# Kernel tuning notes

Measured on AMD Instinct MI355X. Metric: run time of the kernel, lower is better.

Reference implementation:

```python
import jax, jax.numpy as jnp
import numpy as np

N_NODES = 100000
N_EDGES = 3200000
F_IN = 256
N_CLASSES = 10


def setup_inputs() -> dict:
    key = jax.random.key(0)
    ks = jax.random.split(key, 10)
    x = jax.random.normal(ks[0], (N_NODES, F_IN), dtype=jnp.float32)
    edge_index = jax.random.randint(ks[1], (2, N_EDGES), 0, N_NODES, dtype=jnp.int64)
    def glorot(k, fan_in, fan_out):
        s = (6.0 / (fan_in + fan_out)) ** 0.5
        return jax.random.uniform(k, (fan_in, fan_out), jnp.float32, -s, s)
    return {
        "x": x,
        "edge_index": edge_index,
        "W_gcn": glorot(ks[2], F_IN, 64),
        "b_gcn": jnp.zeros((64,), jnp.float32),
        "W1": glorot(ks[3], 64, 32),
        "b1": jnp.zeros((32,), jnp.float32),
        "W2": glorot(ks[4], 32, 16),
        "b2": jnp.zeros((16,), jnp.float32),
        "W3": glorot(ks[5], 16, N_CLASSES),
        "b3": jnp.zeros((N_CLASSES,), jnp.float32),
    }


def gcn_conv(x, edge_index, W, b):
    # PyG GCNConv: x' = D^{-1/2} (A + I) D^{-1/2} (x W) + b, with self-loops.
    n = x.shape[0]
    loop = jnp.arange(n, dtype=edge_index.dtype)
    src = jnp.concatenate([edge_index[0], loop])  # [E+N]
    dst = jnp.concatenate([edge_index[1], loop])
    deg = jax.ops.segment_sum(jnp.ones(src.shape, jnp.float32), dst, num_segments=n)
    dinv = jnp.where(deg > 0, jax.lax.rsqrt(deg), 0.0)
    norm = dinv[src] * dinv[dst]  # [E+N]
    h = x @ W  # transform first (reduces message width to 64)
    msg = h[src] * norm[:, None]  # gather + scale
    out = jax.ops.segment_sum(msg, dst, num_segments=n)  # scatter-add
    return out + b


def reference(x, edge_index, W_gcn, b_gcn, W1, b1, W2, b2, W3, b3):
    # Dropout is a no-op in eval mode; reference uses deterministic eval math.
    h = jax.nn.relu(gcn_conv(x, edge_index, W_gcn, b_gcn))
    h = jax.nn.relu(h @ W1 + b1)
    h = jax.nn.relu(h @ W2 + b2)
    return h @ W3 + b3
```

## Files before the change

kernel.cpp:

```cpp
#include <hip/hip_runtime.h>

#define F_IN 256
#define CHUNK 8192

typedef short bf8_t __attribute__((ext_vector_type(8)));
typedef float f4_t  __attribute__((ext_vector_type(4)));

__device__ __forceinline__ unsigned short f2bf(float f) {
  unsigned u = __float_as_uint(f);
  unsigned r = (u + 0x7FFFu + ((u >> 16) & 1u)) >> 16;
  return (unsigned short)r;
}
#define BF_LO(d) __uint_as_float((d) << 16)
#define BF_HI(d) __uint_as_float((d) & 0xFFFF0000u)

__device__ __forceinline__ bf8_t pack8(float4 a, float4 b) {
  bf8_t r;
  r[0] = (short)f2bf(a.x); r[1] = (short)f2bf(a.y);
  r[2] = (short)f2bf(a.z); r[3] = (short)f2bf(a.w);
  r[4] = (short)f2bf(b.x); r[5] = (short)f2bf(b.y);
  r[6] = (short)f2bf(b.z); r[7] = (short)f2bf(b.w);
  return r;
}

__global__ __launch_bounds__(256) void wprep_kernel(
    const float* __restrict__ W, unsigned short* __restrict__ WbT) {
  const int i = blockIdx.x * 256 + threadIdx.x;
  const int k = i >> 6, n = i & 63;
  WbT[n * 256 + k] = f2bf(W[i]);
}

__global__ __launch_bounds__(256) void gemm_direct_kernel(
    const float* __restrict__ x, const unsigned short* __restrict__ WbT,
    const float* __restrict__ dinvp, unsigned short* __restrict__ hb, int M) {
  __shared__ short Bs[64][264];
  const int t = threadIdx.x;
  for (int i = t; i < 2048; i += 256) {
    const int n = i >> 5, kq = (i & 31) << 3;
    *(uint4*)&Bs[n][kq] = *(const uint4*)(WbT + n * 256 + kq);
  }
  __syncthreads();

  const int brow = blockIdx.x * 128;
  const int w = t >> 6;
  const int l = t & 63;
  const int ml = l & 15;
  const int quad = l >> 4;

  const int r0 = min(brow + w * 32 + ml, M - 1);
  const int r1 = min(brow + w * 32 + 16 + ml, M - 1);
  const float* xr0 = x + (size_t)r0 * F_IN + (quad << 3);
  const float* xr1 = x + (size_t)r1 * F_IN + (quad << 3);

  f4_t acc[2][4];
#pragma unroll
  for (int a = 0; a < 2; ++a)
#pragma unroll
    for (int b = 0; b < 4; ++b) acc[a][b] = (f4_t){0.f, 0.f, 0.f, 0.f};

#pragma unroll
  for (int k0 = 0; k0 < F_IN; k0 += 32) {
    bf8_t afr[2];
    {
      const float4 a0 = *(const float4*)(xr0 + k0);
      const float4 a1 = *(const float4*)(xr0 + k0 + 4);
      afr[0] = pack8(a0, a1);
      const float4 c0 = *(const float4*)(xr1 + k0);
      const float4 c1 = *(const float4*)(xr1 + k0 + 4);
      afr[1] = pack8(c0, c1);
    }
    bf8_t bfr[4];
#pragma unroll
    for (int nt = 0; nt < 4; ++nt)
      bfr[nt] = *(const bf8_t*)&Bs[nt * 16 + ml][k0 + (quad << 3)];
#pragma unroll
    for (int mt = 0; mt < 2; ++mt)
#pragma unroll
      for (int nt = 0; nt < 4; ++nt)
        acc[mt][nt] = __builtin_amdgcn_mfma_f32_16x16x32_bf16(
            afr[mt], bfr[nt], acc[mt][nt], 0, 0, 0);
  }

#pragma unroll
  for (int mt = 0; mt < 2; ++mt) {
#pragma unroll
    for (int reg = 0; reg < 4; ++reg) {
      const int row = brow + w * 32 + mt * 16 + (quad << 2) + reg;
      if (row < M) {
        const float di = dinvp[row];
#pragma unroll
        for (int nt = 0; nt < 4; ++nt)
          hb[(size_t)row * 64 + nt * 16 + ml] = f2bf(di * acc[mt][nt][reg]);
      }
    }
  }
}

__global__ __launch_bounds__(512) void sort_local_kernel(
    const int* __restrict__ src_arr, const int* __restrict__ dst_arr,
    int* __restrict__ espB, int* __restrict__ segStart, int* __restrict__ segCnt,
    int* __restrict__ bucketCount, int E, int NBK) {
  __shared__ int hist[512];
  __shared__ int s[512];
  __shared__ int cur[512];
  const int t = threadIdx.x;
  const int blk = blockIdx.x;
  const int base = blk * CHUNK;
  const int cnt = min(CHUNK, E - base);
  for (int i = t; i < NBK; i += 512) hist[i] = 0;
  __syncthreads();
  int pk[16], bk[16];
#pragma unroll
  for (int k = 0; k < 16; ++k) {
    const int i = t + k * 512;
    bk[k] = -1;
    if (i < cnt) {
      const int sv = src_arr[base + i];
      const int dv = dst_arr[base + i];
      pk[k] = sv | ((dv & 255) << 24);
      bk[k] = dv >> 8;
      atomicAdd(&hist[bk[k]], 1);
    }
  }
  __syncthreads();
  const int v = (t < NBK) ? hist[t] : 0;
  s[t] = v;
  __syncthreads();
#pragma unroll
  for (int off = 1; off < 512; off <<= 1) {
    int add = (t >= off) ? s[t - off] : 0;
    __syncthreads();
    s[t] += add;
    __syncthreads();
  }
  if (t < NBK) {
    const int excl = s[t] - v;
    cur[t] = excl;
    segStart[blk * NBK + t] = base + excl;
    segCnt[blk * NBK + t] = v;
    if (v) atomicAdd(&bucketCount[t], v);
  }
  __syncthreads();
#pragma unroll
  for (int k = 0; k < 16; ++k) {
    if (bk[k] >= 0) {
      const int pos = atomicAdd(&cur[bk[k]], 1);
      espB[base + pos] = pk[k];
    }
  }
}

__global__ __launch_bounds__(512) void scan_buckets_kernel(
    const int* __restrict__ bucketCount, int* __restrict__ bucketStart, int NBK) {
  __shared__ int s[512];
  const int t = threadIdx.x;
  const int v = (t < NBK) ? bucketCount[t] : 0;
  s[t] = v;
  __syncthreads();
#pragma unroll
  for (int off = 1; off < 512; off <<= 1) {
    int add = (t >= off) ? s[t - off] : 0;
    __syncthreads();
    s[t] += add;
    __syncthreads();
  }
  if (t < NBK) bucketStart[t] = s[t] - v;
  if (t == NBK - 1) bucketStart[NBK] = s[t];
}

__global__ __launch_bounds__(512) void fine_bin2_kernel(
    const int* __restrict__ espB, const int* __restrict__ segStart,
    const int* __restrict__ segCnt, const int* __restrict__ bucketStart,
    int* __restrict__ es, int* __restrict__ rowptr, float* __restrict__ dinvp,
    int N, int E, int NBK, int NCH) {
  __shared__ int segS[512];
  __shared__ int segC[512];
  __shared__ int sbuf[512];
  __shared__ int hist[256];
  __shared__ int cur[256];
  const int t = threadIdx.x;
  const int b = blockIdx.x;
  for (int i = t; i < 512; i += 512) { segS[i] = 0; segC[i] = 0; }
  if (t < 256) hist[t] = 0;
  __syncthreads();
  for (int i = t; i < NCH; i += 512) {
    segS[i] = segStart[i * NBK + b];
    segC[i] = segCnt[i * NBK + b];
  }
  __syncthreads();

  const int wid = t >> 6;
  const int lane = t & 63;

  for (int seg = wid; seg < NCH; seg += 8) {
    const int sS = segS[seg], c = segC[seg];
    for (int j = lane; j < c; j += 64)
      atomicAdd(&hist[((unsigned)espB[sS + j]) >> 24], 1);
  }
  __syncthreads();

  int v2 = 0;
  if (t < 256) { v2 = hist[t]; sbuf[t] = v2; }
  __syncthreads();
#pragma unroll
  for (int off = 1; off < 256; off <<= 1) {
    int add = 0;
    if (t < 256 && t >= off) add = sbuf[t - off];
    __syncthreads();
    if (t < 256) sbuf[t] += add;
    __syncthreads();
  }
  const int base = bucketStart[b];
  if (t < 256) {
    const int excl = sbuf[t] - v2;
    cur[t] = base + excl;
    const int node = b * 256 + t;
    if (node < N) {
      rowptr[node] = base + excl;
      dinvp[node] = rsqrtf((float)(v2 + 1));
    }
  }
  if (b == 0 && t == 0) rowptr[N] = E;
  __syncthreads();

  for (int seg = wid; seg < NCH; seg += 8) {
    const int sS = segS[seg], c = segC[seg];
    for (int j = lane; j < c; j += 64) {
      const int p = espB[sS + j];
      const int pos = atomicAdd(&cur[((unsigned)p) >> 24], 1);
      es[pos] = p & 0x00FFFFFF;
    }
  }
}

__global__ __launch_bounds__(256) void agg_csr_kernel(
    const unsigned short* __restrict__ hb, const int* __restrict__ es,
    const int* __restrict__ rowptr, const float* __restrict__ dinvp,
    float* __restrict__ agg, int N) {
  const int t = threadIdx.x;
  const int node = blockIdx.x * 4 + (t >> 6);
  if (node >= N) return;
  const int lane = t & 63;
  const int slot = lane >> 3;
  const int fq = (lane & 7) << 3;
  const int start = rowptr[node];
  const int end = rowptr[node + 1];

  float acc[8] = {0.f};
  int i = start + slot;
  for (; i + 8 < end; i += 16) {
    const int s0 = es[i];
    const int s1 = es[i + 8];
    const uint4 r0 = *(const uint4*)(hb + (size_t)s0 * 64 + fq);
    const uint4 r1 = *(const uint4*)(hb + (size_t)s1 * 64 + fq);
    acc[0] += BF_LO(r0.x) + BF_LO(r1.x);
    acc[1] += BF_HI(r0.x) + BF_HI(r1.x);
    acc[2] += BF_LO(r0.y) + BF_LO(r1.y);
    acc[3] += BF_HI(r0.y) + BF_HI(r1.y);
    acc[4] += BF_LO(r0.z) + BF_LO(r1.z);
    acc[5] += BF_HI(r0.z) + BF_HI(r1.z);
    acc[6] += BF_LO(r0.w) + BF_LO(r1.w);
    acc[7] += BF_HI(r0.w) + BF_HI(r1.w);
  }
  if (i < end) {
    const int s0 = es[i];
    const uint4 r0 = *(const uint4*)(hb + (size_t)s0 * 64 + fq);
    acc[0] += BF_LO(r0.x);
    acc[1] += BF_HI(r0.x);
    acc[2] += BF_LO(r0.y);
    acc[3] += BF_HI(r0.y);
    acc[4] += BF_LO(r0.z);
    acc[5] += BF_HI(r0.z);
    acc[6] += BF_LO(r0.w);
    acc[7] += BF_HI(r0.w);
  }
#pragma unroll
  for (int m = 8; m <= 32; m <<= 1)
#pragma unroll
    for (int j = 0; j < 8; ++j) acc[j] += __shfl_xor(acc[j], m, 64);

  if (slot == 0) {
    const float di = dinvp[node];
    float4 o0 = make_float4(acc[0] * di, acc[1] * di, acc[2] * di, acc[3] * di);
    float4 o1 = make_float4(acc[4] * di, acc[5] * di, acc[6] * di, acc[7] * di);
    float* ap = agg + (size_t)node * 64 + fq;
    *(float4*)(ap + 0) = o0;
    *(float4*)(ap + 4) = o1;
  }
}

__global__ __launch_bounds__(256) void mlp_mfma_kernel(
    const float* __restrict__ agg, const unsigned short* __restrict__ hb,
    const float* __restrict__ dinvp, const float* __restrict__ bg,
    const float* __restrict__ W1, const float* __restrict__ b1,
    const float* __restrict__ W2, const float* __restrict__ b2,
    const float* __restrict__ W3, const float* __restrict__ b3,
    float* __restrict__ out, int N) {
  __shared__ short g64[256 * 72];
  __shared__ short h2s[256 * 40];
  __shared__ short W1s[32 * 72];
  __shared__ short W2s[16 * 40];
  __shared__ short W3s[16 * 40];
  __shared__ float bgs[64], b1s[32], b2s[16], b3s[16];
  short* h1s = g64;

  const int t = threadIdx.x;
  const int node0 = blockIdx.x * 256;
  for (int i = t; i < 256 * 40; i += 256) h2s[i] = 0;
  for (int i = t; i < 16 * 40; i += 256) W3s[i] = 0;
  if (t < 64) bgs[t] = bg[t];
  if (t < 32) b1s[t] = b1[t];
  if (t < 16) { b2s[t] = b2[t]; b3s[t] = (t < 10) ? b3[t] : 0.f; }
  __syncthreads();
  for (int i = t; i < 2048; i += 256) { const int k = i >> 5, n = i & 31; W1s[n * 72 + k] = (short)f2bf(W1[i]); }
  for (int i = t; i < 512;  i += 256) { const int k = i >> 4, n = i & 15; W2s[n * 40 + k] = (short)f2bf(W2[i]); }
  if (t < 160) { const int k = t / 10, n = t % 10; W3s[n * 40 + k] = (short)f2bf(W3[t]); }
  {
    const int nd = min(node0 + t, N - 1);
    const float di = dinvp[nd];
    short* gr = &g64[t * 72];
    const float* ar = agg + (size_t)nd * 64;
    const unsigned short* hr = hb + (size_t)nd * 64;
#pragma unroll
    for (int k = 0; k < 64; k += 8) {
      const float4 a0 = *(const float4*)(ar + k);
      const float4 a1 = *(const float4*)(ar + k + 4);
      const uint4 r = *(const uint4*)(hr + k);
      gr[k + 0] = (short)f2bf(fmaxf(a0.x + di * BF_LO(r.x) + bgs[k + 0], 0.f));
      gr[k + 1] = (short)f2bf(fmaxf(a0.y + di * BF_HI(r.x) + bgs[k + 1], 0.f));
      gr[k + 2] = (short)f2bf(fmaxf(a0.z + di * BF_LO(r.y) + bgs[k + 2], 0.f));
      gr[k + 3] = (short)f2bf(fmaxf(a0.w + di * BF_HI(r.y) + bgs[k + 3], 0.f));
      gr[k + 4] = (short)f2bf(fmaxf(a1.x + di * BF_LO(r.z) + bgs[k + 4], 0.f));
      gr[k + 5] = (short)f2bf(fmaxf(a1.y + di * BF_HI(r.z) + bgs[k + 5], 0.f));
      gr[k + 6] = (short)f2bf(fmaxf(a1.z + di * BF_LO(r.w) + bgs[k + 6], 0.f));
      gr[k + 7] = (short)f2bf(fmaxf(a1.w + di * BF_HI(r.w) + bgs[k + 7], 0.f));
    }
  }
  __syncthreads();

  const int w = t >> 6;
  const int lane = t & 63;
  const int ml = lane & 15;
  const int quad = lane >> 4;

  bf8_t a1f[4][2], b1f[2][2];
#pragma unroll
  for (int mt = 0; mt < 4; ++mt)
#pragma unroll
    for (int ks = 0; ks < 2; ++ks)
      a1f[mt][ks] = *(const bf8_t*)&g64[(w * 64 + mt * 16 + ml) * 72 + ks * 32 + quad * 8];
#pragma unroll
  for (int nt = 0; nt < 2; ++nt)
#pragma unroll
    for (int ks = 0; ks < 2; ++ks)
      b1f[nt][ks] = *(const bf8_t*)&W1s[(nt * 16 + ml) * 72 + ks * 32 + quad * 8];
  f4_t acc1[4][2];
#pragma unroll
  for (int mt = 0; mt < 4; ++mt)
#pragma unroll
    for (int nt = 0; nt < 2; ++nt) acc1[mt][nt] = (f4_t){0.f, 0.f, 0.f, 0.f};
#pragma unroll
  for (int ks = 0; ks < 2; ++ks)
#pragma unroll
    for (int mt = 0; mt < 4; ++mt)
#pragma unroll
      for (int nt = 0; nt < 2; ++nt)
        acc1[mt][nt] = __builtin_amdgcn_mfma_f32_16x16x32_bf16(
            a1f[mt][ks], b1f[nt][ks], acc1[mt][nt], 0, 0, 0);
  __syncthreads();
#pragma unroll
  for (int mt = 0; mt < 4; ++mt)
#pragma unroll
    for (int nt = 0; nt < 2; ++nt)
#pragma unroll
      for (int reg = 0; reg < 4; ++reg) {
        const int row = w * 64 + mt * 16 + quad * 4 + reg;
        const int col = nt * 16 + ml;
        h1s[row * 40 + col] = (short)f2bf(fmaxf(acc1[mt][nt][reg] + b1s[col], 0.f));
      }
  __syncthreads();

  bf8_t a2f[4];
#pragma unroll
  for (int mt = 0; mt < 4; ++mt)
    a2f[mt] = *(const bf8_t*)&h1s[(w * 64 + mt * 16 + ml) * 40 + quad * 8];
  const bf8_t b2f = *(const bf8_t*)&W2s[ml * 40 + quad * 8];
  f4_t acc2[4];
#pragma unroll
  for (int mt = 0; mt < 4; ++mt) {
    acc2[mt] = (f4_t){0.f, 0.f, 0.f, 0.f};
    acc2[mt] = __builtin_amdgcn_mfma_f32_16x16x32_bf16(a2f[mt], b2f, acc2[mt], 0, 0, 0);
  }
  __syncthreads();
#pragma unroll
  for (int mt = 0; mt < 4; ++mt)
#pragma unroll
    for (int reg = 0; reg < 4; ++reg) {
      const int row = w * 64 + mt * 16 + quad * 4 + reg;
      h2s[row * 40 + ml] = (short)f2bf(fmaxf(acc2[mt][reg] + b2s[ml], 0.f));
    }
  __syncthreads();

  bf8_t a3f[4];
#pragma unroll
  for (int mt = 0; mt < 4; ++mt)
    a3f[mt] = *(const bf8_t*)&h2s[(w * 64 + mt * 16 + ml) * 40 + quad * 8];
  const bf8_t b3f = *(const bf8_t*)&W3s[ml * 40 + quad * 8];
#pragma unroll
  for (int mt = 0; mt < 4; ++mt) {
    f4_t acc3 = (f4_t){0.f, 0.f, 0.f, 0.f};
    acc3 = __builtin_amdgcn_mfma_f32_16x16x32_bf16(a3f[mt], b3f, acc3, 0, 0, 0);
#pragma unroll
    for (int reg = 0; reg < 4; ++reg) {
      const int node = node0 + w * 64 + mt * 16 + quad * 4 + reg;
      if (ml < 10 && node < N) out[(size_t)node * 10 + ml] = acc3[reg] + b3s[ml];
    }
  }
}

extern "C" void kernel_launch(void* const* d_in, const int* in_sizes, int n_in,
                              void* d_out, int out_size, void* d_ws, size_t ws_size,
                              hipStream_t stream) {
  const float* x     = (const float*)d_in[0];
  const int*   ei    = (const int*)d_in[1];
  const float* W_gcn = (const float*)d_in[2];
  const float* b_gcn = (const float*)d_in[3];
  const float* W1    = (const float*)d_in[4];
  const float* b1    = (const float*)d_in[5];
  const float* W2    = (const float*)d_in[6];
  const float* b2    = (const float*)d_in[7];
  const float* W3    = (const float*)d_in[8];
  const float* b3    = (const float*)d_in[9];
  float* out = (float*)d_out;

  const int N = in_sizes[0] / F_IN;
  const int E = in_sizes[1] / 2;
  const int* src = ei;
  const int* dst = ei + E;
  const int NBK = (N + 255) >> 8;
  const int NCH = (E + CHUNK - 1) / CHUNK;

  unsigned short* hb = (unsigned short*)d_ws;
  float* dinvp       = (float*)(hb + (size_t)N * 64);
  int*   es          = (int*)(dinvp + N);
  int*   rowptr      = es + E;
  int*   bucketCount = rowptr + N + 16;
  int*   bucketStart = bucketCount + 512;
  int*   espB        = bucketStart + 528;
  int*   segStart    = espB + E;
  int*   segCnt      = segStart + NCH * NBK;
  unsigned short* WbT= (unsigned short*)(segCnt + NCH * NBK);
  float* agg         = (float*)espB;

  hipMemsetAsync(bucketCount, 0, 512 * sizeof(int), stream);

  wprep_kernel<<<64, 256, 0, stream>>>(W_gcn, WbT);
  sort_local_kernel<<<NCH, 512, 0, stream>>>(
      src, dst, espB, segStart, segCnt, bucketCount, E, NBK);
  scan_buckets_kernel<<<1, 512, 0, stream>>>(bucketCount, bucketStart, NBK);
  fine_bin2_kernel<<<NBK, 512, 0, stream>>>(
      espB, segStart, segCnt, bucketStart, es, rowptr, dinvp, N, E, NBK, NCH);

  gemm_direct_kernel<<<(N + 127) / 128, 256, 0, stream>>>(x, WbT, dinvp, hb, N);

  agg_csr_kernel<<<(N + 3) / 4, 256, 0, stream>>>(hb, es, rowptr, dinvp, agg, N);

  mlp_mfma_kernel<<<(N + 255) / 256, 256, 0, stream>>>(
      agg, hb, dinvp, b_gcn, W1, b1, W2, b2, W3, b3, out, N);
}
```

Baseline: 342.2 us.

## Fuse per-bucket CSR build, aggregation and MLP into one kernel

Drops the global CSR construction (bucket-count atomics, bucket scan, global es/rowptr arrays) and the separate aggregation and MLP kernels. One 1024-thread block per 256-node bucket now rebuilds its local CSR in LDS from the locally sorted edge segments, gathers neighbour features, adds the self loop and bias with ReLU, and runs the three MFMA MLP layers without writing the fp32 agg buffer to global memory. A small kernel still computes degrees for the GEMM prescale. The cost is recomputing degrees in the fused kernel, heavy LDS use that allows only one block per CU with few blocks in flight, and a fixed edge-list capacity per bucket with no overflow check.

```diff
diff --git a/kernel.cpp b/kernel.cpp
--- a/kernel.cpp
+++ b/kernel.cpp
@@ -2,6 +2,7 @@
 
 #define F_IN 256
 #define CHUNK 8192
+#define ESL_CAP 10240
 
 typedef short bf8_t __attribute__((ext_vector_type(8)));
 typedef float f4_t  __attribute__((ext_vector_type(4)));
@@ -99,7 +100,7 @@
 __global__ __launch_bounds__(512) void sort_local_kernel(
     const int* __restrict__ src_arr, const int* __restrict__ dst_arr,
     int* __restrict__ espB, int* __restrict__ segStart, int* __restrict__ segCnt,
-    int* __restrict__ bucketCount, int E, int NBK) {
+    int E, int NBK) {
   __shared__ int hist[512];
   __shared__ int s[512];
   __shared__ int cur[512];
@@ -138,7 +139,6 @@
     cur[t] = excl;
     segStart[blk * NBK + t] = base + excl;
     segCnt[blk * NBK + t] = v;
-    if (v) atomicAdd(&bucketCount[t], v);
   }
   __syncthreads();
 #pragma unroll
@@ -150,57 +150,84 @@
   }
 }
 
-__global__ __launch_bounds__(512) void scan_buckets_kernel(
-    const int* __restrict__ bucketCount, int* __restrict__ bucketStart, int NBK) {
-  __shared__ int s[512];
-  const int t = threadIdx.x;
-  const int v = (t < NBK) ? bucketCount[t] : 0;
-  s[t] = v;
-  __syncthreads();
-#pragma unroll
-  for (int off = 1; off < 512; off <<= 1) {
-    int add = (t >= off) ? s[t - off] : 0;
-    __syncthreads();
-    s[t] += add;
-    __syncthreads();
-  }
-  if (t < NBK) bucketStart[t] = s[t] - v;
-  if (t == NBK - 1) bucketStart[NBK] = s[t];
-}
-
-__global__ __launch_bounds__(512) void fine_bin2_kernel(
+__global__ __launch_bounds__(512) void deg_seg_kernel(
     const int* __restrict__ espB, const int* __restrict__ segStart,
-    const int* __restrict__ segCnt, const int* __restrict__ bucketStart,
-    int* __restrict__ es, int* __restrict__ rowptr, float* __restrict__ dinvp,
-    int N, int E, int NBK, int NCH) {
+    const int* __restrict__ segCnt, float* __restrict__ dinvp,
+    int N, int NBK, int NCH) {
   __shared__ int segS[512];
   __shared__ int segC[512];
-  __shared__ int sbuf[512];
   __shared__ int hist[256];
-  __shared__ int cur[256];
   const int t = threadIdx.x;
   const int b = blockIdx.x;
-  for (int i = t; i < 512; i += 512) { segS[i] = 0; segC[i] = 0; }
   if (t < 256) hist[t] = 0;
+  if (t < 512) { segS[t] = 0; segC[t] = 0; }
   __syncthreads();
   for (int i = t; i < NCH; i += 512) {
     segS[i] = segStart[i * NBK + b];
     segC[i] = segCnt[i * NBK + b];
   }
   __syncthreads();
-
-  const int wid = t >> 6;
-  const int lane = t & 63;
-
+  const int wid = t >> 6, lane = t & 63;
   for (int seg = wid; seg < NCH; seg += 8) {
     const int sS = segS[seg], c = segC[seg];
     for (int j = lane; j < c; j += 64)
       atomicAdd(&hist[((unsigned)espB[sS + j]) >> 24], 1);
   }
   __syncthreads();
-
-  int v2 = 0;
-  if (t < 256) { v2 = hist[t]; sbuf[t] = v2; }
+  const int node = b * 256 + t;
+  if (t < 256 && node < N) dinvp[node] = rsqrtf((float)(hist[t] + 1));
+}
+
+__global__ __launch_bounds__(1024) void fused_agg_mlp_kernel(
+    const unsigned short* __restrict__ hb, const int* __restrict__ espB,
+    const int* __restrict__ segStart, const int* __restrict__ segCnt,
+    const float* __restrict__ bg,
+    const float* __restrict__ W1, const float* __restrict__ b1,
+    const float* __restrict__ W2, const float* __restrict__ b2,
+    const float* __restrict__ W3, const float* __restrict__ b3,
+    float* __restrict__ out, int N, int NBK, int NCH) {
+  __shared__ int esL[ESL_CAP];
+  __shared__ short g64[256 * 72];
+  __shared__ short h2s[256 * 40];
+  __shared__ short W1s[32 * 72];
+  __shared__ short W2s[16 * 40];
+  __shared__ short W3s[16 * 40];
+  __shared__ int segS[512], segC[512];
+  __shared__ int deg[256], rp[257], cur[256], sbuf[256];
+  __shared__ float bgs[64], b1s[32], b2s[16], b3s[16];
+  short* h1s = g64;
+
+  const int t = threadIdx.x;
+  const int b = blockIdx.x;
+  const int node0 = b * 256;
+
+  for (int i = t; i < 256 * 40; i += 1024) h2s[i] = 0;
+  for (int i = t; i < 16 * 40; i += 1024) W3s[i] = 0;
+  if (t < 256) deg[t] = 0;
+  if (t < 512) { segS[t] = 0; segC[t] = 0; }
+  if (t < 64) bgs[t] = bg[t];
+  if (t < 32) b1s[t] = b1[t];
+  if (t < 16) { b2s[t] = b2[t]; b3s[t] = (t < 10) ? b3[t] : 0.f; }
+  for (int i = t; i < NCH; i += 1024) {
+    segS[i] = segStart[i * NBK + b];
+    segC[i] = segCnt[i * NBK + b];
+  }
+  for (int i = t; i < 2048; i += 1024) { const int k = i >> 5, n = i & 31; W1s[n * 72 + k] = (short)f2bf(W1[i]); }
+  for (int i = t; i < 512;  i += 1024) { const int k = i >> 4, n = i & 15; W2s[n * 40 + k] = (short)f2bf(W2[i]); }
+  if (t < 160) { const int k = t / 10, n = t % 10; W3s[n * 40 + k] = (short)f2bf(W3[t]); }
+  __syncthreads();
+
+  const int wid = t >> 6, lane = t & 63;
+
+  for (int seg = wid; seg < NCH; seg += 16) {
+    const int sS = segS[seg], c = segC[seg];
+    for (int j = lane; j < c; j += 64)
+      atomicAdd(&deg[((unsigned)espB[sS + j]) >> 24], 1);
+  }
+  __syncthreads();
+
+  int v = 0;
+  if (t < 256) { v = deg[t]; sbuf[t] = v; }
   __syncthreads();
 #pragma unroll
   for (int off = 1; off < 256; off <<= 1) {
@@ -210,211 +237,130 @@
     if (t < 256) sbuf[t] += add;
     __syncthreads();
   }
-  const int base = bucketStart[b];
-  if (t < 256) {
-    const int excl = sbuf[t] - v2;
-    cur[t] = base + excl;
-    const int node = b * 256 + t;
-    if (node < N) {
-      rowptr[node] = base + excl;
-      dinvp[node] = rsqrtf((float)(v2 + 1));
-    }
-  }
-  if (b == 0 && t == 0) rowptr[N] = E;
-  __syncthreads();
-
-  for (int seg = wid; seg < NCH; seg += 8) {
+  if (t < 256) { rp[t] = sbuf[t] - v; cur[t] = sbuf[t] - v; }
+  if (t == 255) rp[256] = sbuf[255];
+  __syncthreads();
+
+  for (int seg = wid; seg < NCH; seg += 16) {
     const int sS = segS[seg], c = segC[seg];
     for (int j = lane; j < c; j += 64) {
       const int p = espB[sS + j];
       const int pos = atomicAdd(&cur[((unsigned)p) >> 24], 1);
-      es[pos] = p & 0x00FFFFFF;
-    }
-  }
-}
-
-__global__ __launch_bounds__(256) void agg_csr_kernel(
-    const unsigned short* __restrict__ hb, const int* __restrict__ es,
-    const int* __restrict__ rowptr, const float* __restrict__ dinvp,
-    float* __restrict__ agg, int N) {
-  const int t = threadIdx.x;
-  const int node = blockIdx.x * 4 + (t >> 6);
-  if (node >= N) return;
-  const int lane = t & 63;
+      esL[pos] = p & 0x00FFFFFF;
+    }
+  }
+  __syncthreads();
+
   const int slot = lane >> 3;
   const int fq = (lane & 7) << 3;
-  const int start = rowptr[node];
-  const int end = rowptr[node + 1];
-
-  float acc[8] = {0.f};
-  int i = start + slot;
-  for (; i + 8 < end; i += 16) {
-    const int s0 = es[i];
-    const int s1 = es[i + 8];
-    const uint4 r0 = *(const uint4*)(hb + (size_t)s0 * 64 + fq);
-    const uint4 r1 = *(const uint4*)(hb + (size_t)s1 * 64 + fq);
-    acc[0] += BF_LO(r0.x) + BF_LO(r1.x);
-    acc[1] += BF_HI(r0.x) + BF_HI(r1.x);
-    acc[2] += BF_LO(r0.y) + BF_LO(r1.y);
-    acc[3] += BF_HI(r0.y) + BF_HI(r1.y);
-    acc[4] += BF_LO(r0.z) + BF_LO(r1.z);
-    acc[5] += BF_HI(r0.z) + BF_HI(r1.z);
-    acc[6] += BF_LO(r0.w) + BF_LO(r1.w);
-    acc[7] += BF_HI(r0.w) + BF_HI(r1.w);
-  }
-  if (i < end) {
-    const int s0 = es[i];
-    const uint4 r0 = *(const uint4*)(hb + (size_t)s0 * 64 + fq);
-    acc[0] += BF_LO(r0.x);
-    acc[1] += BF_HI(r0.x);
-    acc[2] += BF_LO(r0.y);
-    acc[3] += BF_HI(r0.y);
-    acc[4] += BF_LO(r0.z);
-    acc[5] += BF_HI(r0.z);
-    acc[6] += BF_LO(r0.w);
-    acc[7] += BF_HI(r0.w);
-  }
-#pragma unroll
-  for (int m = 8; m <= 32; m <<= 1)
-#pragma unroll
-    for (int j = 0; j < 8; ++j) acc[j] += __shfl_xor(acc[j], m, 64);
-
-  if (slot == 0) {
-    const float di = dinvp[node];
-    float4 o0 = make_float4(acc[0] * di, acc[1] * di, acc[2] * di, acc[3] * di);
-    float4 o1 = make_float4(acc[4] * di, acc[5] * di, acc[6] * di, acc[7] * di);
-    float* ap = agg + (size_t)node * 64 + fq;
-    *(float4*)(ap + 0) = o0;
-    *(float4*)(ap + 4) = o1;
-  }
-}
-
-__global__ __launch_bounds__(256) void mlp_mfma_kernel(
-    const float* __restrict__ agg, const unsigned short* __restrict__ hb,
-    const float* __restrict__ dinvp, const float* __restrict__ bg,
-    const float* __restrict__ W1, const float* __restrict__ b1,
-    const float* __restrict__ W2, const float* __restrict__ b2,
-    const float* __restrict__ W3, const float* __restrict__ b3,
-    float* __restrict__ out, int N) {
-  __shared__ short g64[256 * 72];
-  __shared__ short h2s[256 * 40];
-  __shared__ short W1s[32 * 72];
-  __shared__ short W2s[16 * 40];
-  __shared__ short W3s[16 * 40];
-  __shared__ float bgs[64], b1s[32], b2s[16], b3s[16];
-  short* h1s = g64;
-
-  const int t = threadIdx.x;
-  const int node0 = blockIdx.x * 256;
-  for (int i = t; i < 256 * 40; i += 256) h2s[i] = 0;
-  for (int i = t; i < 16 * 40; i += 256) W3s[i] = 0;
-  if (t < 64) bgs[t] = bg[t];
-  if (t < 32) b1s[t] = b1[t];
-  if (t < 16) { b2s[t] = b2[t]; b3s[t] = (t < 10) ? b3[t] : 0.f; }
-  __syncthreads();
-  for (int i = t; i < 2048; i += 256) { const int k = i >> 5, n = i & 31; W1s[n * 72 + k] = (short)f2bf(W1[i]); }
-  for (int i = t; i < 512;  i += 256) { const int k = i >> 4, n = i & 15; W2s[n * 40 + k] = (short)f2bf(W2[i]); }
-  if (t < 160) { const int k = t / 10, n = t % 10; W3s[n * 40 + k] = (short)f2bf(W3[t]); }
-  {
-    const int nd = min(node0 + t, N - 1);
-    const float di = dinvp[nd];
-    short* gr = &g64[t * 72];
-    const float* ar = agg + (size_t)nd * 64;
-    const unsigned short* hr = hb + (size_t)nd * 64;
-#pragma unroll
-    for (int k = 0; k < 64; k += 8) {
-      const float4 a0 = *(const float4*)(ar + k);
-      const float4 a1 = *(const float4*)(ar + k + 4);
-      const uint4 r = *(const uint4*)(hr + k);
-      gr[k + 0] = (short)f2bf(fmaxf(a0.x + di * BF_LO(r.x) + bgs[k + 0], 0.f));
-      gr[k + 1] = (short)f2bf(fmaxf(a0.y + di * BF_HI(r.x) + bgs[k + 1], 0.f));
-      gr[k + 2] = (short)f2bf(fmaxf(a0.z + di * BF_LO(r.y) + bgs[k + 2], 0.f));
-      gr[k + 3] = (short)f2bf(fmaxf(a0.w + di * BF_HI(r.y) + bgs[k + 3], 0.f));
-      gr[k + 4] = (short)f2bf(fmaxf(a1.x + di * BF_LO(r.z) + bgs[k + 4], 0.f));
-      gr[k + 5] = (short)f2bf(fmaxf(a1.y + di * BF_HI(r.z) + bgs[k + 5], 0.f));
-      gr[k + 6] = (short)f2bf(fmaxf(a1.z + di * BF_LO(r.w) + bgs[k + 6], 0.f));
-      gr[k + 7] = (short)f2bf(fmaxf(a1.w + di * BF_HI(r.w) + bgs[k + 7], 0.f));
-    }
-  }
-  __syncthreads();
-
-  const int w = t >> 6;
-  const int lane = t & 63;
+  for (int node = wid; node < 256; node += 16) {
+    const int start = rp[node];
+    const int end = rp[node + 1];
+    float acc[8] = {0.f};
+    int i = start + slot;
+    for (; i + 8 < end; i += 16) {
+      const int s0 = esL[i];
+      const int s1 = esL[i + 8];
+      const uint4 r0 = *(const uint4*)(hb + (size_t)s0 * 64 + fq);
+      const uint4 r1 = *(const uint4*)(hb + (size_t)s1 * 64 + fq);
+      acc[0] += BF_LO(r0.x) + BF_LO(r1.x);
+      acc[1] += BF_HI(r0.x) + BF_HI(r1.x);
+      acc[2] += BF_LO(r0.y) + BF_LO(r1.y);
+      acc[3] += BF_HI(r0.y) + BF_HI(r1.y);
+      acc[4] += BF_LO(r0.z) + BF_LO(r1.z);
+      acc[5] += BF_HI(r0.z) + BF_HI(r1.z);
+      acc[6] += BF_LO(r0.w) + BF_LO(r1.w);
+      acc[7] += BF_HI(r0.w) + BF_HI(r1.w);
+    }
+    if (i < end) {
+      const int s0 = esL[i];
+      const uint4 r0 = *(const uint4*)(hb + (size_t)s0 * 64 + fq);
+      acc[0] += BF_LO(r0.x);
+      acc[1] += BF_HI(r0.x);
+      acc[2] += BF_LO(r0.y);
+      acc[3] += BF_HI(r0.y);
+      acc[4] += BF_LO(r0.z);
+      acc[5] += BF_HI(r0.z);
+      acc[6] += BF_LO(r0.w);
+      acc[7] += BF_HI(r0.w);
+    }
+#pragma unroll
+    for (int m = 8; m <= 32; m <<= 1)
+#pragma unroll
+      for (int j = 0; j < 8; ++j) acc[j] += __shfl_xor(acc[j], m, 64);
+
+    if (slot == 0) {
+      const int gn = node0 + node;
+      if (gn < N) {
+        const uint4 r = *(const uint4*)(hb + (size_t)gn * 64 + fq);
+        acc[0] += BF_LO(r.x); acc[1] += BF_HI(r.x);
+        acc[2] += BF_LO(r.y); acc[3] += BF_HI(r.y);
+        acc[4] += BF_LO(r.z); acc[5] += BF_HI(r.z);
+        acc[6] += BF_LO(r.w); acc[7] += BF_HI(r.w);
+      }
+      const float di = rsqrtf((float)(deg[node] + 1));
+      bf8_t g;
+#pragma unroll
+      for (int j = 0; j < 8; ++j)
+        g[j] = (short)f2bf(fmaxf(di * acc[j] + bgs[fq + j], 0.f));
+      *(bf8_t*)&g64[node * 72 + fq] = g;
+    }
+  }
+  __syncthreads();
+
+  const int rb = wid * 16;
   const int ml = lane & 15;
   const int quad = lane >> 4;
 
-  bf8_t a1f[4][2], b1f[2][2];
-#pragma unroll
-  for (int mt = 0; mt < 4; ++mt)
-#pragma unroll
-    for (int ks = 0; ks < 2; ++ks)
-      a1f[mt][ks] = *(const bf8_t*)&g64[(w * 64 + mt * 16 + ml) * 72 + ks * 32 + quad * 8];
+  bf8_t a1f[2], b1f[2][2];
+#pragma unroll
+  for (int ks = 0; ks < 2; ++ks)
+    a1f[ks] = *(const bf8_t*)&g64[(rb + ml) * 72 + ks * 32 + quad * 8];
 #pragma unroll
   for (int nt = 0; nt < 2; ++nt)
 #pragma unroll
     for (int ks = 0; ks < 2; ++ks)
       b1f[nt][ks] = *(const bf8_t*)&W1s[(nt * 16 + ml) * 72 + ks * 32 + quad * 8];
-  f4_t acc1[4][2];
-#pragma unroll
-  for (int mt = 0; mt < 4; ++mt)
-#pragma unroll
-    for (int nt = 0; nt < 2; ++nt) acc1[mt][nt] = (f4_t){0.f, 0.f, 0.f, 0.f};
+  f4_t acc1[2];
+#pragma unroll
+  for (int nt = 0; nt < 2; ++nt) acc1[nt] = (f4_t){0.f, 0.f, 0.f, 0.f};
 #pragma unroll
   for (int ks = 0; ks < 2; ++ks)
 #pragma unroll
-    for (int mt = 0; mt < 4; ++mt)
-#pragma unroll
-      for (int nt = 0; nt < 2; ++nt)
-        acc1[mt][nt] = __builtin_amdgcn_mfma_f32_16x16x32_bf16(
-            a1f[mt][ks], b1f[nt][ks], acc1[mt][nt], 0, 0, 0);
-  __syncthreads();
-#pragma unroll
-  for (int mt = 0; mt < 4; ++mt)
-#pragma unroll
     for (int nt = 0; nt < 2; ++nt)
-#pragma unroll
-      for (int reg = 0; reg < 4; ++reg) {
-        const int row = w * 64 + mt * 16 + quad * 4 + reg;
-        const int col = nt * 16 + ml;
-        h1s[row * 40 + col] = (short)f2bf(fmaxf(acc1[mt][nt][reg] + b1s[col], 0.f));
-      }
-  __syncthreads();
-
-  bf8_t a2f[4];
-#pragma unroll
-  for (int mt = 0; mt < 4; ++mt)
-    a2f[mt] = *(const bf8_t*)&h1s[(w * 64 + mt * 16 + ml) * 40 + quad * 8];
+      acc1[nt] = __builtin_amdgcn_mfma_f32_16x16x32_bf16(
+          a1f[ks], b1f[nt][ks], acc1[nt], 0, 0, 0);
+  __syncthreads();
+#pragma unroll
+  for (int nt = 0; nt < 2; ++nt)
+#pragma unroll
+    for (int reg = 0; reg < 4; ++reg) {
+      const int row = rb + quad * 4 + reg;
+      const int col = nt * 16 + ml;
+      h1s[row * 40 + col] = (short)f2bf(fmaxf(acc1[nt][reg] + b1s[col], 0.f));
+    }
+  __syncthreads();
+
+  const bf8_t a2f = *(const bf8_t*)&h1s[(rb + ml) * 40 + quad * 8];
   const bf8_t b2f = *(const bf8_t*)&W2s[ml * 40 + quad * 8];
-  f4_t acc2[4];
-#pragma unroll
-  for (int mt = 0; mt < 4; ++mt) {
-    acc2[mt] = (f4_t){0.f, 0.f, 0.f, 0.f};
-    acc2[mt] = __builtin_amdgcn_mfma_f32_16x16x32_bf16(a2f[mt], b2f, acc2[mt], 0, 0, 0);
-  }
-  __syncthreads();
-#pragma unroll
-  for (int mt = 0; mt < 4; ++mt)
-#pragma unroll
-    for (int reg = 0; reg < 4; ++reg) {
-      const int row = w * 64 + mt * 16 + quad * 4 + reg;
-      h2s[row * 40 + ml] = (short)f2bf(fmaxf(acc2[mt][reg] + b2s[ml], 0.f));
-    }
-  __syncthreads();
-
-  bf8_t a3f[4];
-#pragma unroll
-  for (int mt = 0; mt < 4; ++mt)
-    a3f[mt] = *(const bf8_t*)&h2s[(w * 64 + mt * 16 + ml) * 40 + quad * 8];
+  f4_t acc2 = (f4_t){0.f, 0.f, 0.f, 0.f};
+  acc2 = __builtin_amdgcn_mfma_f32_16x16x32_bf16(a2f, b2f, acc2, 0, 0, 0);
+  __syncthreads();
+#pragma unroll
+  for (int reg = 0; reg < 4; ++reg) {
+    const int row = rb + quad * 4 + reg;
+    h2s[row * 40 + ml] = (short)f2bf(fmaxf(acc2[reg] + b2s[ml], 0.f));
+  }
+  __syncthreads();
+
+  const bf8_t a3f = *(const bf8_t*)&h2s[(rb + ml) * 40 + quad * 8];
   const bf8_t b3f = *(const bf8_t*)&W3s[ml * 40 + quad * 8];
-#pragma unroll
-  for (int mt = 0; mt < 4; ++mt) {
-    f4_t acc3 = (f4_t){0.f, 0.f, 0.f, 0.f};
-    acc3 = __builtin_amdgcn_mfma_f32_16x16x32_bf16(a3f[mt], b3f, acc3, 0, 0, 0);
-#pragma unroll
-    for (int reg = 0; reg < 4; ++reg) {
-      const int node = node0 + w * 64 + mt * 16 + quad * 4 + reg;
-      if (ml < 10 && node < N) out[(size_t)node * 10 + ml] = acc3[reg] + b3s[ml];
-    }
+  f4_t acc3 = (f4_t){0.f, 0.f, 0.f, 0.f};
+  acc3 = __builtin_amdgcn_mfma_f32_16x16x32_bf16(a3f, b3f, acc3, 0, 0, 0);
+#pragma unroll
+  for (int reg = 0; reg < 4; ++reg) {
+    const int node = node0 + rb + quad * 4 + reg;
+    if (ml < 10 && node < N) out[(size_t)node * 10 + ml] = acc3[reg] + b3s[ml];
   }
 }
 
@@ -442,29 +388,15 @@
 
   unsigned short* hb = (unsigned short*)d_ws;
   float* dinvp       = (float*)(hb + (size_t)N * 64);
-  int*   es          = (int*)(dinvp + N);
-  int*   rowptr      = es + E;
-  int*   bucketCount = rowptr + N + 16;
-  int*   bucketStart = bucketCount + 512;
-  int*   espB        = bucketStart + 528;
+  int*   espB        = (int*)(dinvp + N);
   int*   segStart    = espB + E;
   int*   segCnt      = segStart + NCH * NBK;
   unsigned short* WbT= (unsigned short*)(segCnt + NCH * NBK);
-  float* agg         = (float*)espB;
-
-  hipMemsetAsync(bucketCount, 0, 512 * sizeof(int), stream);
 
   wprep_kernel<<<64, 256, 0, stream>>>(W_gcn, WbT);
-  sort_local_kernel<<<NCH, 512, 0, stream>>>(
-      src, dst, espB, segStart, segCnt, bucketCount, E, NBK);
-  scan_buckets_kernel<<<1, 512, 0, stream>>>(bucketCount, bucketStart, NBK);
-  fine_bin2_kernel<<<NBK, 512, 0, stream>>>(
-      espB, segStart, segCnt, bucketStart, es, rowptr, dinvp, N, E, NBK, NCH);
-
+  sort_local_kernel<<<NCH, 512, 0, stream>>>(src, dst, espB, segStart, segCnt, E, NBK);
+  deg_seg_kernel<<<NBK, 512, 0, stream>>>(espB, segStart, segCnt, dinvp, N, NBK, NCH);
   gemm_direct_kernel<<<(N + 127) / 128, 256, 0, stream>>>(x, WbT, dinvp, hb, N);
-
-  agg_csr_kernel<<<(N + 3) / 4, 256, 0, stream>>>(hb, es, rowptr, dinvp, agg, N);
-
-  mlp_mfma_kernel<<<(N + 255) / 256, 256, 0, stream>>>(
-      agg, hb, dinvp, b_gcn, W1, b1, W2, b2, W3, b3, out, N);
-}
+  fused_agg_mlp_kernel<<<NBK, 1024, 0, stream>>>(
+      hb, espB, segStart, segCnt, b_gcn, W1, b1, W2, b2, W3, b3, out, N, NBK, NCH);
+}
```

New measurement: 363.2 us. 6.1% more time.
